# Kernel optimization log

Hardware: AMD Instinct MI355X
Metric: run time of the kernel (lower is better)

## Reference

```python
import jax, jax.numpy as jnp
import numpy as np

B, T, D, H = 4, 2048, 1024, 16
HD = D // H


def setup_inputs() -> dict:
    key = jax.random.key(0)
    ks = jax.random.split(key, 10)
    s = 1.0 / np.sqrt(D)
    # xavier_uniform bound for wbias [T,T]: sqrt(6/(T+T))
    wb_bound = float(np.sqrt(6.0 / (T + T)))
    return {
        "x": jax.random.normal(ks[0], (B, T, D), dtype=jnp.float32),
        "Wq": jax.random.normal(ks[1], (D, D), dtype=jnp.float32) * s,
        "bq": jnp.zeros((D,), dtype=jnp.float32),
        "Wk": jax.random.normal(ks[2], (D, D), dtype=jnp.float32) * s,
        "bk": jnp.zeros((D,), dtype=jnp.float32),
        "Wv": jax.random.normal(ks[3], (D, D), dtype=jnp.float32) * s,
        "bv": jnp.zeros((D,), dtype=jnp.float32),
        "Wo": jax.random.normal(ks[4], (D, D), dtype=jnp.float32) * s,
        "bo": jnp.zeros((D,), dtype=jnp.float32),
        "wbias": jax.random.uniform(ks[5], (T, T), dtype=jnp.float32,
                                    minval=-wb_bound, maxval=wb_bound),
    }


def reference(x, Wq, bq, Wk, bk, Wv, bv, Wo, bo, wbias):
    Bc, Tc, Dc = x.shape
    # projections, split heads: [B, H, T, HD]
    def proj(W, b):
        y = x @ W + b
        return y.reshape(Bc, Tc, H, HD).transpose(0, 2, 1, 3)

    Q = proj(Wq, bq)
    K = proj(Wk, bk)
    V = proj(Wv, bv)

    Q_sig = jax.nn.sigmoid(Q)
    eK = jnp.exp(K)                      # [B,H,T,HD]
    ew = jnp.exp(wbias[:Tc, :Tc])        # [T,T]

    num = jnp.einsum('ts,bhsd->bhtd', ew, eK * V)
    den = jnp.einsum('ts,bhsd->bhtd', ew, eK)
    out = Q_sig * (num / den)            # [B,H,T,HD]

    out = out.transpose(0, 2, 1, 3).reshape(Bc, Tc, Dc)
    return out @ Wo + bo
```

## Files before the change

kernel.cpp:

```cpp
#include <hip/hip_runtime.h>
#include <hip/hip_bf16.h>


#define AS1(p) ((const __attribute__((address_space(1))) void*)(p))
#define AS3(p) ((__attribute__((address_space(3))) void*)(p))

typedef _Float16 half8 __attribute__((ext_vector_type(8)));
typedef _Float16 half4v __attribute__((ext_vector_type(4)));
typedef float floatx16 __attribute__((ext_vector_type(16)));
typedef int intx4 __attribute__((ext_vector_type(4)));
typedef int intx8 __attribute__((ext_vector_type(8)));

__device__ __forceinline__ long frag_off(int r, int k) {
  return (long)(((((r >> 5) * 4 + (k >> 4)) * 2 + ((k >> 3) & 1)) * 32 + (r & 31)) * 8 + (k & 7));
}
__device__ __forceinline__ long off8(int r, int k) {
  return (long)((((((r >> 5) * 2 + ((k >> 6) & 1)) * 2 + ((k >> 4) & 1)) * 2 + ((k >> 5) & 1)) * 32 +
                 (r & 31)) * 16 + (k & 15));
}

__global__ __launch_bounds__(256) void prep_all(
    const float* __restrict__ x, const float* __restrict__ wb, const float* __restrict__ Wq,
    const float* __restrict__ Wk, const float* __restrict__ Wv, const float* __restrict__ Wo,
    _Float16* __restrict__ x_h, char* __restrict__ E8, _Float16* __restrict__ WqkvT,
    _Float16* __restrict__ WoT) {
  __shared__ _Float16 lds[64 * 132];
  const int bid = blockIdx.x;
  const int tid = threadIdx.x;

  if (bid < 1024) {
    const int tm = bid >> 4, tk = bid & 15;
    const long tbase = (long)bid * 8192;
#pragma unroll
    for (int p = 0; p < 4; ++p) {
      const int s = p * 256 + tid;
      const int r = ((s >> 8) << 5) + (s & 31);
      const int k = ((s >> 6) & 3) * 16 + ((s >> 5) & 1) * 8;
      const float* sp = x + (long)(tm * 128 + r) * 1024 + tk * 64 + k;
      const float4 v0 = *(const float4*)sp;
      const float4 v1 = *(const float4*)(sp + 4);
      half8 h;
      h[0] = (_Float16)v0.x; h[1] = (_Float16)v0.y; h[2] = (_Float16)v0.z; h[3] = (_Float16)v0.w;
      h[4] = (_Float16)v1.x; h[5] = (_Float16)v1.y; h[6] = (_Float16)v1.z; h[7] = (_Float16)v1.w;
      *(half8*)(x_h + tbase + (long)s * 8) = h;
    }
    return;
  }

  if (bid >= 1536) {
    const int e = bid - 1536;
    const int tt = e >> 4, ts = e & 15;
    char* dst = E8 + (long)e * 16384;
#pragma unroll
    for (int p = 0; p < 16; ++p) {
      const int idx = p * 256 + tid;
      const int r = idx >> 5, k = (idx & 31) * 4;
      const float4 v = *(const float4*)(wb + (long)(tt * 128 + r) * 2048 + ts * 128 + k);
      const float e0 = (__expf(v.x) - 1.0f) * 32.0f, e1 = (__expf(v.y) - 1.0f) * 32.0f;
      const float e2 = (__expf(v.z) - 1.0f) * 32.0f, e3 = (__expf(v.w) - 1.0f) * 32.0f;
      int pk = __builtin_amdgcn_cvt_pk_fp8_f32(e0, e1, 0, false);
      pk = __builtin_amdgcn_cvt_pk_fp8_f32(e2, e3, pk, true);
      *(int*)(dst + off8(r, k)) = pk;
    }
    return;
  }

  const int b2 = bid - 1024;
  const float* src0;
  const float* src1 = nullptr;
  _Float16* dst;
  int tn, tk, cb = 0;
  if (b2 < 128) {
    tn = b2 >> 4; tk = b2 & 15; src0 = Wq; dst = WqkvT;
  } else if (b2 < 384) {
    const int t = b2 - 128;
    tn = 8 + (t >> 4); tk = t & 15; cb = (tn - 8) * 64; src0 = Wk; src1 = Wv; dst = WqkvT;
  } else {
    const int t = b2 - 384;
    tn = t >> 4; tk = t & 15; src0 = Wo; dst = WoT;
  }
  if (!src1) {
#pragma unroll
    for (int p = 0; p < 8; ++p) {
      const int kl = p * 8 + (tid >> 5);
      const int cl = (tid & 31) * 4;
      const float4 v = *(const float4*)(src0 + (long)(tk * 64 + kl) * 1024 + tn * 128 + cl);
      half4v h;
      h[0] = (_Float16)v.x; h[1] = (_Float16)v.y; h[2] = (_Float16)v.z; h[3] = (_Float16)v.w;
      *(half4v*)(lds + kl * 132 + cl) = h;
    }
  } else {
#pragma unroll
    for (int m = 0; m < 2; ++m) {
      const float* s = m ? src1 : src0;
      const int rb = m ? 32 : 0;
#pragma unroll
      for (int p = 0; p < 4; ++p) {
        const int kl = p * 16 + (tid >> 4);
        const int cl = (tid & 15) * 4;
        const int rl = (cl >> 5) * 64 + rb + (cl & 31);
        const float4 v = *(const float4*)(s + (long)(tk * 64 + kl) * 1024 + cb + cl);
        half4v h;
        h[0] = (_Float16)v.x; h[1] = (_Float16)v.y; h[2] = (_Float16)v.z; h[3] = (_Float16)v.w;
        *(half4v*)(lds + kl * 132 + rl) = h;
      }
    }
  }
  __syncthreads();
  const long tbase = (long)(tn * 16 + tk) * 8192;
#pragma unroll
  for (int p = 0; p < 4; ++p) {
    const int s = p * 256 + tid;
    const int r = ((s >> 8) << 5) + (s & 31);
    const int kl = ((s >> 6) & 3) * 16 + ((s >> 5) & 1) * 8;
    half8 h;
#pragma unroll
    for (int j = 0; j < 8; ++j) h[j] = lds[(kl + j) * 132 + r];
    *(half8*)(dst + tbase + (long)s * 8) = h;
  }
}

template <int VM, bool STAGE>
__device__ __forceinline__ void aft_phase2(
    const _Float16* rA, const _Float16* rB, _Float16* sAd, _Float16* sBd,
    const _Float16* gA, const _Float16* gB, int lane, int wm, int wn,
    floatx16 (&acc)[2][4]) {
  half8 af[2][2], bf[4][2];
#pragma unroll
  for (int mt = 0; mt < 2; ++mt)
#pragma unroll
    for (int ks = 0; ks < 2; ++ks)
      af[mt][ks] = *(const half8*)(rA + (((wm >> 5) + mt) * 2 + ks) * 512 + lane * 8);
#pragma unroll
  for (int nt = 0; nt < 4; ++nt)
#pragma unroll
    for (int ks = 0; ks < 2; ++ks)
      bf[nt][ks] = *(const half8*)(rB + (((wn >> 5) + nt) * 2 + ks) * 512 + lane * 8);
  if (STAGE) {
#pragma unroll
    for (int p = 0; p < 2; ++p)
      __builtin_amdgcn_global_load_lds(AS1(gA + p * 4096), AS3(sAd + p * 2048), 16, 0, 0);
#pragma unroll
    for (int q = 0; q < 4; ++q)
      __builtin_amdgcn_global_load_lds(AS1(gB + (q >> 1) * 131072 + (q & 1) * 4096),
                                       AS3(sBd + q * 2048), 16, 0, 0);
  }
  asm volatile("s_waitcnt lgkmcnt(0)" ::: "memory");
  __builtin_amdgcn_s_setprio(1);
#pragma unroll
  for (int ks = 0; ks < 2; ++ks)
#pragma unroll
    for (int mt = 0; mt < 2; ++mt)
#pragma unroll
      for (int nt = 0; nt < 4; ++nt)
        acc[mt][nt] =
            __builtin_amdgcn_mfma_f32_32x32x16_f16(af[mt][ks], bf[nt][ks], acc[mt][nt], 0, 0, 0);
  __builtin_amdgcn_s_setprio(0);
  asm volatile("s_waitcnt vmcnt(%0)" ::"i"(VM) : "memory");
  __builtin_amdgcn_s_barrier();
  asm volatile("" ::: "memory");
}

template <int MODE>
__global__ __launch_bounds__(256, 2) void gemm_bt2(
    const _Float16* __restrict__ A, const _Float16* __restrict__ Bt, void* __restrict__ Cv,
    const float* __restrict__ bias0, const float* __restrict__ bias1,
    const float* __restrict__ bias2, char* __restrict__ Zt8, float* __restrict__ cs) {
  __shared__ __align__(16) _Float16 ring[36864];
  const int tid = threadIdx.x;
  const int wid = tid >> 6, lane = tid & 63;
  const int l32 = lane & 31, khalf = lane >> 5;

  const int f = blockIdx.x;
  const int j = f >> 3;
  const int bxs = (f & 7) * 8 + (j & 7);
  const int bys = j >> 3;
  const int m0 = bxs * 128, n0 = bys * 256;
  const int wm = (wid >> 1) * 64, wn = (wid & 1) * 128;

  const long thrOff = (long)(tid >> 7) * 2048 + (tid & 127) * 8;
  const _Float16* gA0 = A + (long)bxs * 131072 + thrOff;
  const _Float16* gB0 = Bt + (long)(bys * 2) * 131072 + thrOff;

  _Float16* ringB = ring + 12288;
  _Float16* sAt = ring + tid * 8;
  _Float16* sBt = ringB + tid * 8;

#pragma unroll
  for (int ph = 0; ph < 2; ++ph) {
    const _Float16* ga = gA0 + ph * 1024;
    const _Float16* gb = gB0 + ph * 1024;
#pragma unroll
    for (int p = 0; p < 2; ++p)
      __builtin_amdgcn_global_load_lds(AS1(ga + p * 4096), AS3(sAt + ph * 4096 + p * 2048), 16, 0, 0);
#pragma unroll
    for (int q = 0; q < 4; ++q)
      __builtin_amdgcn_global_load_lds(AS1(gb + (q >> 1) * 131072 + (q & 1) * 4096),
                                       AS3(sBt + ph * 8192 + q * 2048), 16, 0, 0);
  }
  asm volatile("s_waitcnt vmcnt(6)" ::: "memory");
  __builtin_amdgcn_s_barrier();
  asm volatile("" ::: "memory");

  floatx16 acc[2][4] = {};

#pragma unroll
  for (int pr = 0; pr < 15; ++pr) {
    const int s0 = (2 * pr) % 3, s1 = (2 * pr + 1) % 3, s2 = (2 * pr + 2) % 3;
    const _Float16* gA = gA0 + (long)(pr + 1) * 8192;
    const _Float16* gB = gB0 + (long)(pr + 1) * 8192;
    aft_phase2<6, true>(ring + s0 * 4096, ringB + s0 * 8192, sAt + s2 * 4096, sBt + s2 * 8192,
                        gA, gB, lane, wm, wn, acc);
    aft_phase2<6, true>(ring + s1 * 4096, ringB + s1 * 8192, sAt + s0 * 4096, sBt + s0 * 8192,
                        gA + 1024, gB + 1024, lane, wm, wn, acc);
  }
  aft_phase2<0, false>(ring + 0 * 4096, ringB + 0 * 8192, nullptr, nullptr, nullptr, nullptr,
                       lane, wm, wn, acc);
  aft_phase2<0, false>(ring + 1 * 4096, ringB + 1 * 8192, nullptr, nullptr, nullptr, nullptr,
                       lane, wm, wn, acc);

  if (MODE == 0) {
    if (n0 < 1024) {
      _Float16* Qs = (_Float16*)Cv;
#pragma unroll
      for (int mt = 0; mt < 2; ++mt) {
        const long ttile = (m0 + wm + mt * 32) >> 5;
#pragma unroll
        for (int nt = 0; nt < 4; ++nt) {
          const int col = n0 + wn + nt * 32 + l32;
          const float bb = bias0[col];
          const long base = (ttile * 32 + (((n0 + wn) >> 5) + nt)) * 1024;
#pragma unroll
          for (int q = 0; q < 4; ++q) {
            half4v o;
#pragma unroll
            for (int rr = 0; rr < 4; ++rr) {
              const float v = acc[mt][nt][q * 4 + rr] + bb;
              o[rr] = (_Float16)(1.0f / (1.0f + __expf(-v)));
            }
            *(half4v*)(Qs + base + q * 256 + lane * 4) = o;
          }
        }
      }
    } else {
      const int b = m0 >> 11;
      const int g0 = (n0 - 1024 + wn) >> 6;
#pragma unroll
      for (int p = 0; p < 2; ++p) {
        const int grp = g0 + p;
        const int ch = grp * 32 + l32;
        const float bkc = bias1[ch], bvc = bias2[ch];
        const int jn = grp * 64 + l32;
        char* Z8 = Zt8 + (long)b * 4194304 +
                   ((long)(jn >> 7) * 16 + ((m0 & 2047) >> 7)) * 16384;
        const int jnl = jn & 127;
        float sk = 0.f, sz = 0.f;
#pragma unroll
        for (int mt = 0; mt < 2; ++mt) {
#pragma unroll
          for (int q = 0; q < 4; ++q) {
            float ekv[4], ekk[4];
#pragma unroll
            for (int rr = 0; rr < 4; ++rr) {
              const float ek = __expf(acc[mt][2 * p][q * 4 + rr] + bkc);
              const float vv = acc[mt][2 * p + 1][q * 4 + rr] + bvc;
              ekk[rr] = ek;
              ekv[rr] = ek * vv;
              sk += ek;
              sz += ek * vv;
            }
            const int sl = wm + mt * 32 + 4 * khalf + 8 * q;
            int pn = __builtin_amdgcn_cvt_pk_fp8_f32(ekv[0] * 0.25f, ekv[1] * 0.25f, 0, false);
            pn = __builtin_amdgcn_cvt_pk_fp8_f32(ekv[2] * 0.25f, ekv[3] * 0.25f, pn, true);
            int pd = __builtin_amdgcn_cvt_pk_fp8_f32(ekk[0] * 0.25f, ekk[1] * 0.25f, 0, false);
            pd = __builtin_amdgcn_cvt_pk_fp8_f32(ekk[2] * 0.25f, ekk[3] * 0.25f, pd, true);
            *(int*)(Z8 + off8(jnl, sl)) = pn;
            *(int*)(Z8 + off8(jnl + 32, sl)) = pd;
          }
        }
        atomicAdd(&cs[(long)b * 2048 + ch * 2], sz);
        atomicAdd(&cs[(long)b * 2048 + ch * 2 + 1], sk);
      }
    }
    return;
  }

#pragma unroll
  for (int mt = 0; mt < 2; ++mt)
#pragma unroll
    for (int nt = 0; nt < 4; ++nt) {
      const int col = n0 + wn + nt * 32 + l32;
      const float bb = bias0[col];
#pragma unroll
      for (int reg = 0; reg < 16; ++reg) {
        const int row = m0 + wm + mt * 32 + 4 * khalf + 8 * (reg >> 2) + (reg & 3);
        ((float*)Cv)[(long)row * 1024 + col] = acc[mt][nt][reg] + bb;
      }
    }
}

__global__ __launch_bounds__(256) void gemm2_fp8(
    const char* __restrict__ E8, const char* __restrict__ Zt8, _Float16* __restrict__ OH,
    const _Float16* __restrict__ Qsig, const float* __restrict__ cs) {
  __shared__ __align__(16) char sA[16384];
  __shared__ __align__(16) char sB[16384];
  const int tid = threadIdx.x;
  const int wave = tid >> 6, lane = tid & 63;
  const int l32 = lane & 31, khalf = lane >> 5;

  const int f = blockIdx.x + 16 * (blockIdx.y + 16 * blockIdx.z);
  const int nid = (f & 7) * 128 + (f >> 3);
  const int bxs = nid & 15, bys = (nid >> 4) & 15, bzs = nid >> 8;

  const int m0 = bxs * 128, n0 = bys * 128;
  const int wm = (wave >> 1) * 64, wn = (wave & 1) * 64;

  const char* At = E8 + (long)bxs * 16 * 16384;
  const char* Bt = Zt8 + (long)bzs * 4194304 + (long)bys * 16 * 16384;

  floatx16 acc[2][2] = {};

  for (int tk = 0; tk < 16; ++tk) {
    const char* As = At + tk * 16384 + wave * 1024 + lane * 16;
    const char* Bs = Bt + tk * 16384 + wave * 1024 + lane * 16;
#pragma unroll
    for (int c = 0; c < 4; ++c) {
      __builtin_amdgcn_global_load_lds(AS1(As + c * 4096), AS3(sA + c * 4096 + wave * 1024), 16, 0, 0);
      __builtin_amdgcn_global_load_lds(AS1(Bs + c * 4096), AS3(sB + c * 4096 + wave * 1024), 16, 0, 0);
    }
    __syncthreads();
#pragma unroll
    for (int ks = 0; ks < 2; ++ks) {
      intx8 a8[2], b8[2];
#pragma unroll
      for (int i = 0; i < 2; ++i) {
        const char* pa = sA + (((wm >> 5) + i) * 2 + ks) * 2048 + khalf * 512 + l32 * 16;
        const intx4 alo = *(const intx4*)pa;
        const intx4 ahi = *(const intx4*)(pa + 1024);
        a8[i] = __builtin_shufflevector(alo, ahi, 0, 1, 2, 3, 4, 5, 6, 7);
        const char* pb = sB + (((wn >> 5) + i) * 2 + ks) * 2048 + khalf * 512 + l32 * 16;
        const intx4 blo = *(const intx4*)pb;
        const intx4 bhi = *(const intx4*)(pb + 1024);
        b8[i] = __builtin_shufflevector(blo, bhi, 0, 1, 2, 3, 4, 5, 6, 7);
      }
#pragma unroll
      for (int mt = 0; mt < 2; ++mt)
#pragma unroll
        for (int nt = 0; nt < 2; ++nt)
          acc[mt][nt] = __builtin_amdgcn_mfma_scale_f32_32x32x64_f8f6f4(
              a8[mt], b8[nt], acc[mt][nt], 0, 0, 0, 127u, 0, 127u);
    }
    __syncthreads();
  }

  const int ch = ((n0 + wn) >> 6) * 32 + l32;
  const float2 c2 = *(const float2*)(cs + (long)bzs * 2048 + ch * 2);
#pragma unroll
  for (int mt = 0; mt < 2; ++mt) {
    const long ttile = (long)(bzs * 2048 + m0 + wm + mt * 32) >> 5;
    const long qbase = (ttile * 32 + ((n0 + wn) >> 6)) * 1024;
#pragma unroll
    for (int q = 0; q < 4; ++q) {
      const half4v qv = *(const half4v*)(Qsig + qbase + q * 256 + lane * 4);
#pragma unroll
      for (int rr = 0; rr < 4; ++rr) {
        const int reg = q * 4 + rr;
        const float num = c2.x + acc[mt][0][reg] * 0.125f;
        const float den = c2.y + acc[mt][1][reg] * 0.125f;
        const int r = m0 + wm + mt * 32 + 4 * khalf + 8 * q + rr;
        const int R = bzs * 2048 + r;
        const long off = ((long)(R >> 7) * 16 + (ch >> 6)) * 8192 + frag_off(R & 127, ch & 63);
        OH[off] = (_Float16)((float)qv[rr] * num / den);
      }
    }
  }
}

extern "C" void kernel_launch(void* const* d_in, const int* in_sizes, int n_in, void* d_out,
                              int out_size, void* d_ws, size_t ws_size, hipStream_t stream) {
  const float* x = (const float*)d_in[0];
  const float* Wq = (const float*)d_in[1];
  const float* bq = (const float*)d_in[2];
  const float* Wk = (const float*)d_in[3];
  const float* bk = (const float*)d_in[4];
  const float* Wv = (const float*)d_in[5];
  const float* bv = (const float*)d_in[6];
  const float* Wo = (const float*)d_in[7];
  const float* bo = (const float*)d_in[8];
  const float* wb = (const float*)d_in[9];

  char* ws = (char*)d_ws;
  _Float16* x_h = (_Float16*)(ws + 0);
  _Float16* WqkvT = (_Float16*)(ws + 16777216);
  _Float16* WoT = (_Float16*)(ws + 23068672);
  char* E8 = (char*)(ws + 25165824);
  _Float16* Qsig = (_Float16*)(ws + 29360128);
  char* Zt8 = (char*)(ws + 46137344);
  _Float16* OutHead = (_Float16*)(ws + 62914560);
  float* cs = (float*)(ws + 79691776);

  hipMemsetAsync(cs, 0, 4 * 2048 * sizeof(float), stream);

  prep_all<<<1792, 256, 0, stream>>>(x, wb, Wq, Wk, Wv, Wo, x_h, E8, WqkvT, WoT);

  gemm_bt2<0><<<768, 256, 0, stream>>>(x_h, WqkvT, Qsig, bq, bk, bv, Zt8, cs);

  gemm2_fp8<<<dim3(16, 16, 4), 256, 0, stream>>>(E8, Zt8, OutHead, Qsig, cs);

  gemm_bt2<2><<<256, 256, 0, stream>>>(OutHead, WoT, d_out, bo, nullptr, nullptr, nullptr, nullptr);
}
```

Before: 251.1 us.

## Swap GEMM tile to 256x128 with 4-slot ring and register double-buffered fragments

The projection GEMM kernel changes its block tile from 128x256 to 256x128, with each wave now covering 128x64. It moves from a 3-slot to a 4-slot LDS ring, and fragments for the next k-slice are loaded into registers while the current MFMAs run, which removes the lgkmcnt(0) stall before each compute step. Launch bounds drop to one block per CU to leave room for the larger LDS ring and more registers. This aims to hide LDS latency, at the cost of lower occupancy and a reworked epilogue mapping, especially the fp8 K/V tile indexing.

```diff
diff --git a/kernel.cpp b/kernel.cpp
--- a/kernel.cpp
+++ b/kernel.cpp
@@ -120,122 +120,133 @@
   }
 }
 
-template <int VM, bool STAGE>
-__device__ __forceinline__ void aft_phase2(
-    const _Float16* rA, const _Float16* rB, _Float16* sAd, _Float16* sBd,
-    const _Float16* gA, const _Float16* gB, int lane, int wm, int wn,
-    floatx16 (&acc)[2][4]) {
-  half8 af[2][2], bf[4][2];
-#pragma unroll
-  for (int mt = 0; mt < 2; ++mt)
-#pragma unroll
-    for (int ks = 0; ks < 2; ++ks)
-      af[mt][ks] = *(const half8*)(rA + (((wm >> 5) + mt) * 2 + ks) * 512 + lane * 8);
-#pragma unroll
-  for (int nt = 0; nt < 4; ++nt)
-#pragma unroll
-    for (int ks = 0; ks < 2; ++ks)
-      bf[nt][ks] = *(const half8*)(rB + (((wn >> 5) + nt) * 2 + ks) * 512 + lane * 8);
+template <int VM, bool STAGE, bool LOADNEXT>
+__device__ __forceinline__ void aft_phase3(
+    const int g, _Float16* __restrict__ ring, _Float16* __restrict__ ringB,
+    const _Float16* gA0, const _Float16* gA1, const _Float16* gB,
+    const int tid, const int lane, const int wm, const int wn,
+    half8 (&afc)[4], half8 (&bfc)[2], floatx16 (&acc)[4][2]) {
+  const int slot = g & 3, nslot = (g + 1) & 3, sslot = (g + 3) & 3;
+  const _Float16* rA = ring + slot * 8192 + (wm >> 7) * 4096 + lane * 8;
+  const _Float16* rB = ringB + slot * 4096 + (wn >> 5) * 1024 + lane * 8;
+  half8 afn[4], bfn[2];
+#pragma unroll
+  for (int mf = 0; mf < 4; ++mf) afn[mf] = *(const half8*)(rA + mf * 1024 + 512);
+#pragma unroll
+  for (int nf = 0; nf < 2; ++nf) bfn[nf] = *(const half8*)(rB + nf * 1024 + 512);
   if (STAGE) {
-#pragma unroll
-    for (int p = 0; p < 2; ++p)
-      __builtin_amdgcn_global_load_lds(AS1(gA + p * 4096), AS3(sAd + p * 2048), 16, 0, 0);
-#pragma unroll
-    for (int q = 0; q < 4; ++q)
-      __builtin_amdgcn_global_load_lds(AS1(gB + (q >> 1) * 131072 + (q & 1) * 4096),
-                                       AS3(sBd + q * 2048), 16, 0, 0);
-  }
-  asm volatile("s_waitcnt lgkmcnt(0)" ::: "memory");
+    const long soff = (long)((g + 3) >> 1) * 8192 + (long)((g + 3) & 1) * 1024;
+    _Float16* dA = ring + sslot * 8192 + tid * 8;
+    _Float16* dB = ringB + sslot * 4096 + tid * 8;
+#pragma unroll
+    for (int p = 0; p < 2; ++p) {
+      __builtin_amdgcn_global_load_lds(AS1(gA0 + soff + p * 4096), AS3(dA + p * 2048), 16, 0, 0);
+      __builtin_amdgcn_global_load_lds(AS1(gA1 + soff + p * 4096), AS3(dA + 4096 + p * 2048), 16, 0, 0);
+      __builtin_amdgcn_global_load_lds(AS1(gB + soff + p * 4096), AS3(dB + p * 2048), 16, 0, 0);
+    }
+  }
   __builtin_amdgcn_s_setprio(1);
 #pragma unroll
-  for (int ks = 0; ks < 2; ++ks)
-#pragma unroll
-    for (int mt = 0; mt < 2; ++mt)
-#pragma unroll
-      for (int nt = 0; nt < 4; ++nt)
-        acc[mt][nt] =
-            __builtin_amdgcn_mfma_f32_32x32x16_f16(af[mt][ks], bf[nt][ks], acc[mt][nt], 0, 0, 0);
+  for (int mf = 0; mf < 4; ++mf)
+#pragma unroll
+    for (int nf = 0; nf < 2; ++nf)
+      acc[mf][nf] = __builtin_amdgcn_mfma_f32_32x32x16_f16(afc[mf], bfc[nf], acc[mf][nf], 0, 0, 0);
   __builtin_amdgcn_s_setprio(0);
-  asm volatile("s_waitcnt vmcnt(%0)" ::"i"(VM) : "memory");
-  __builtin_amdgcn_s_barrier();
-  asm volatile("" ::: "memory");
+  if (LOADNEXT) {
+    const _Float16* rA2 = ring + nslot * 8192 + (wm >> 7) * 4096 + lane * 8;
+    const _Float16* rB2 = ringB + nslot * 4096 + (wn >> 5) * 1024 + lane * 8;
+#pragma unroll
+    for (int mf = 0; mf < 4; ++mf) afc[mf] = *(const half8*)(rA2 + mf * 1024);
+#pragma unroll
+    for (int nf = 0; nf < 2; ++nf) bfc[nf] = *(const half8*)(rB2 + nf * 1024);
+  }
+  __builtin_amdgcn_s_setprio(1);
+#pragma unroll
+  for (int mf = 0; mf < 4; ++mf)
+#pragma unroll
+    for (int nf = 0; nf < 2; ++nf)
+      acc[mf][nf] = __builtin_amdgcn_mfma_f32_32x32x16_f16(afn[mf], bfn[nf], acc[mf][nf], 0, 0, 0);
+  __builtin_amdgcn_s_setprio(0);
+  if constexpr (VM >= 0) {
+    asm volatile("s_waitcnt vmcnt(%0)" ::"i"(VM) : "memory");
+    __builtin_amdgcn_s_barrier();
+    asm volatile("" ::: "memory");
+  }
 }
 
 template <int MODE>
-__global__ __launch_bounds__(256, 2) void gemm_bt2(
+__global__ __launch_bounds__(256, 1) void gemm_bt2(
     const _Float16* __restrict__ A, const _Float16* __restrict__ Bt, void* __restrict__ Cv,
     const float* __restrict__ bias0, const float* __restrict__ bias1,
     const float* __restrict__ bias2, char* __restrict__ Zt8, float* __restrict__ cs) {
-  __shared__ __align__(16) _Float16 ring[36864];
+  __shared__ __align__(16) _Float16 ring[49152];
+  _Float16* ringB = ring + 32768;
   const int tid = threadIdx.x;
   const int wid = tid >> 6, lane = tid & 63;
   const int l32 = lane & 31, khalf = lane >> 5;
 
   const int f = blockIdx.x;
-  const int j = f >> 3;
-  const int bxs = (f & 7) * 8 + (j & 7);
-  const int bys = j >> 3;
-  const int m0 = bxs * 128, n0 = bys * 256;
-  const int wm = (wid >> 1) * 64, wn = (wid & 1) * 128;
+  const int bxs = (f & 7) * 4 + ((f >> 3) & 3);
+  const int bys = f >> 5;
+  const int m0 = bxs * 256, n0 = bys * 128;
+  const int wm = (wid >> 1) * 128, wn = (wid & 1) * 64;
 
   const long thrOff = (long)(tid >> 7) * 2048 + (tid & 127) * 8;
-  const _Float16* gA0 = A + (long)bxs * 131072 + thrOff;
-  const _Float16* gB0 = Bt + (long)(bys * 2) * 131072 + thrOff;
-
-  _Float16* ringB = ring + 12288;
-  _Float16* sAt = ring + tid * 8;
-  _Float16* sBt = ringB + tid * 8;
-
-#pragma unroll
-  for (int ph = 0; ph < 2; ++ph) {
-    const _Float16* ga = gA0 + ph * 1024;
-    const _Float16* gb = gB0 + ph * 1024;
-#pragma unroll
-    for (int p = 0; p < 2; ++p)
-      __builtin_amdgcn_global_load_lds(AS1(ga + p * 4096), AS3(sAt + ph * 4096 + p * 2048), 16, 0, 0);
-#pragma unroll
-    for (int q = 0; q < 4; ++q)
-      __builtin_amdgcn_global_load_lds(AS1(gb + (q >> 1) * 131072 + (q & 1) * 4096),
-                                       AS3(sBt + ph * 8192 + q * 2048), 16, 0, 0);
+  const _Float16* gA0 = A + (long)(bxs * 2) * 131072 + thrOff;
+  const _Float16* gA1 = gA0 + 131072;
+  const _Float16* gB = Bt + (long)bys * 131072 + thrOff;
+
+#pragma unroll
+  for (int hh = 0; hh < 3; ++hh) {
+    const long soff = (long)(hh >> 1) * 8192 + (long)(hh & 1) * 1024;
+    _Float16* dA = ring + hh * 8192 + tid * 8;
+    _Float16* dB = ringB + hh * 4096 + tid * 8;
+#pragma unroll
+    for (int p = 0; p < 2; ++p) {
+      __builtin_amdgcn_global_load_lds(AS1(gA0 + soff + p * 4096), AS3(dA + p * 2048), 16, 0, 0);
+      __builtin_amdgcn_global_load_lds(AS1(gA1 + soff + p * 4096), AS3(dA + 4096 + p * 2048), 16, 0, 0);
+      __builtin_amdgcn_global_load_lds(AS1(gB + soff + p * 4096), AS3(dB + p * 2048), 16, 0, 0);
+    }
   }
   asm volatile("s_waitcnt vmcnt(6)" ::: "memory");
   __builtin_amdgcn_s_barrier();
   asm volatile("" ::: "memory");
 
-  floatx16 acc[2][4] = {};
-
-#pragma unroll
-  for (int pr = 0; pr < 15; ++pr) {
-    const int s0 = (2 * pr) % 3, s1 = (2 * pr + 1) % 3, s2 = (2 * pr + 2) % 3;
-    const _Float16* gA = gA0 + (long)(pr + 1) * 8192;
-    const _Float16* gB = gB0 + (long)(pr + 1) * 8192;
-    aft_phase2<6, true>(ring + s0 * 4096, ringB + s0 * 8192, sAt + s2 * 4096, sBt + s2 * 8192,
-                        gA, gB, lane, wm, wn, acc);
-    aft_phase2<6, true>(ring + s1 * 4096, ringB + s1 * 8192, sAt + s0 * 4096, sBt + s0 * 8192,
-                        gA + 1024, gB + 1024, lane, wm, wn, acc);
-  }
-  aft_phase2<0, false>(ring + 0 * 4096, ringB + 0 * 8192, nullptr, nullptr, nullptr, nullptr,
-                       lane, wm, wn, acc);
-  aft_phase2<0, false>(ring + 1 * 4096, ringB + 1 * 8192, nullptr, nullptr, nullptr, nullptr,
-                       lane, wm, wn, acc);
+  half8 afc[4], bfc[2];
+  {
+    const _Float16* rA = ring + (wm >> 7) * 4096 + lane * 8;
+    const _Float16* rB = ringB + (wn >> 5) * 1024 + lane * 8;
+#pragma unroll
+    for (int mf = 0; mf < 4; ++mf) afc[mf] = *(const half8*)(rA + mf * 1024);
+#pragma unroll
+    for (int nf = 0; nf < 2; ++nf) bfc[nf] = *(const half8*)(rB + nf * 1024);
+  }
+
+  floatx16 acc[4][2] = {};
+#pragma unroll
+  for (int g = 0; g < 29; ++g)
+    aft_phase3<6, true, true>(g, ring, ringB, gA0, gA1, gB, tid, lane, wm, wn, afc, bfc, acc);
+  aft_phase3<0, false, true>(29, ring, ringB, gA0, gA1, gB, tid, lane, wm, wn, afc, bfc, acc);
+  aft_phase3<-1, false, true>(30, ring, ringB, gA0, gA1, gB, tid, lane, wm, wn, afc, bfc, acc);
+  aft_phase3<-1, false, false>(31, ring, ringB, gA0, gA1, gB, tid, lane, wm, wn, afc, bfc, acc);
 
   if (MODE == 0) {
     if (n0 < 1024) {
       _Float16* Qs = (_Float16*)Cv;
 #pragma unroll
-      for (int mt = 0; mt < 2; ++mt) {
-        const long ttile = (m0 + wm + mt * 32) >> 5;
-#pragma unroll
-        for (int nt = 0; nt < 4; ++nt) {
-          const int col = n0 + wn + nt * 32 + l32;
+      for (int mf = 0; mf < 4; ++mf) {
+        const long ttile = (m0 + wm + mf * 32) >> 5;
+#pragma unroll
+        for (int nf = 0; nf < 2; ++nf) {
+          const int col = n0 + wn + nf * 32 + l32;
           const float bb = bias0[col];
-          const long base = (ttile * 32 + (((n0 + wn) >> 5) + nt)) * 1024;
+          const long base = (ttile * 32 + ((n0 + wn) >> 5) + nf) * 1024;
 #pragma unroll
           for (int q = 0; q < 4; ++q) {
             half4v o;
 #pragma unroll
             for (int rr = 0; rr < 4; ++rr) {
-              const float v = acc[mt][nt][q * 4 + rr] + bb;
+              const float v = acc[mf][nf][q * 4 + rr] + bb;
               o[rr] = (_Float16)(1.0f / (1.0f + __expf(-v)));
             }
             *(half4v*)(Qs + base + q * 256 + lane * 4) = o;
@@ -244,57 +255,53 @@
       }
     } else {
       const int b = m0 >> 11;
-      const int g0 = (n0 - 1024 + wn) >> 6;
-#pragma unroll
-      for (int p = 0; p < 2; ++p) {
-        const int grp = g0 + p;
-        const int ch = grp * 32 + l32;
-        const float bkc = bias1[ch], bvc = bias2[ch];
-        const int jn = grp * 64 + l32;
-        char* Z8 = Zt8 + (long)b * 4194304 +
-                   ((long)(jn >> 7) * 16 + ((m0 & 2047) >> 7)) * 16384;
-        const int jnl = jn & 127;
-        float sk = 0.f, sz = 0.f;
-#pragma unroll
-        for (int mt = 0; mt < 2; ++mt) {
-#pragma unroll
-          for (int q = 0; q < 4; ++q) {
-            float ekv[4], ekk[4];
-#pragma unroll
-            for (int rr = 0; rr < 4; ++rr) {
-              const float ek = __expf(acc[mt][2 * p][q * 4 + rr] + bkc);
-              const float vv = acc[mt][2 * p + 1][q * 4 + rr] + bvc;
-              ekk[rr] = ek;
-              ekv[rr] = ek * vv;
-              sk += ek;
-              sz += ek * vv;
-            }
-            const int sl = wm + mt * 32 + 4 * khalf + 8 * q;
-            int pn = __builtin_amdgcn_cvt_pk_fp8_f32(ekv[0] * 0.25f, ekv[1] * 0.25f, 0, false);
-            pn = __builtin_amdgcn_cvt_pk_fp8_f32(ekv[2] * 0.25f, ekv[3] * 0.25f, pn, true);
-            int pd = __builtin_amdgcn_cvt_pk_fp8_f32(ekk[0] * 0.25f, ekk[1] * 0.25f, 0, false);
-            pd = __builtin_amdgcn_cvt_pk_fp8_f32(ekk[2] * 0.25f, ekk[3] * 0.25f, pd, true);
-            *(int*)(Z8 + off8(jnl, sl)) = pn;
-            *(int*)(Z8 + off8(jnl + 32, sl)) = pd;
+      const int grp = (n0 - 1024 + wn) >> 6;
+      const int ch = grp * 32 + l32;
+      const float bkc = bias1[ch], bvc = bias2[ch];
+      const int jn = grp * 64 + l32;
+      const int tc = ((m0 & 2047) >> 7) + (wm >> 7);
+      char* Z8 = Zt8 + (long)b * 4194304 + ((long)(jn >> 7) * 16 + tc) * 16384;
+      const int jnl = jn & 127;
+      float sk = 0.f, sz = 0.f;
+#pragma unroll
+      for (int mf = 0; mf < 4; ++mf) {
+#pragma unroll
+        for (int q = 0; q < 4; ++q) {
+          float ekv[4], ekk[4];
+#pragma unroll
+          for (int rr = 0; rr < 4; ++rr) {
+            const float ek = __expf(acc[mf][0][q * 4 + rr] + bkc);
+            const float vv = acc[mf][1][q * 4 + rr] + bvc;
+            ekk[rr] = ek;
+            ekv[rr] = ek * vv;
+            sk += ek;
+            sz += ek * vv;
           }
+          const int sl = mf * 32 + 4 * khalf + 8 * q;
+          int pn = __builtin_amdgcn_cvt_pk_fp8_f32(ekv[0] * 0.25f, ekv[1] * 0.25f, 0, false);
+          pn = __builtin_amdgcn_cvt_pk_fp8_f32(ekv[2] * 0.25f, ekv[3] * 0.25f, pn, true);
+          int pd = __builtin_amdgcn_cvt_pk_fp8_f32(ekk[0] * 0.25f, ekk[1] * 0.25f, 0, false);
+          pd = __builtin_amdgcn_cvt_pk_fp8_f32(ekk[2] * 0.25f, ekk[3] * 0.25f, pd, true);
+          *(int*)(Z8 + off8(jnl, sl)) = pn;
+          *(int*)(Z8 + off8(jnl + 32, sl)) = pd;
         }
-        atomicAdd(&cs[(long)b * 2048 + ch * 2], sz);
-        atomicAdd(&cs[(long)b * 2048 + ch * 2 + 1], sk);
-      }
+      }
+      atomicAdd(&cs[(long)b * 2048 + ch * 2], sz);
+      atomicAdd(&cs[(long)b * 2048 + ch * 2 + 1], sk);
     }
     return;
   }
 
 #pragma unroll
-  for (int mt = 0; mt < 2; ++mt)
-#pragma unroll
-    for (int nt = 0; nt < 4; ++nt) {
-      const int col = n0 + wn + nt * 32 + l32;
+  for (int mf = 0; mf < 4; ++mf)
+#pragma unroll
+    for (int nf = 0; nf < 2; ++nf) {
+      const int col = n0 + wn + nf * 32 + l32;
       const float bb = bias0[col];
 #pragma unroll
       for (int reg = 0; reg < 16; ++reg) {
-        const int row = m0 + wm + mt * 32 + 4 * khalf + 8 * (reg >> 2) + (reg & 3);
-        ((float*)Cv)[(long)row * 1024 + col] = acc[mt][nt][reg] + bb;
+        const int row = m0 + wm + mf * 32 + 4 * khalf + 8 * (reg >> 2) + (reg & 3);
+        ((float*)Cv)[(long)row * 1024 + col] = acc[mf][nf][reg] + bb;
       }
     }
 }
```

New measurement: 276.2 us. 1.1x slower.
